# Performance work log

Measured on AMD Instinct MI355X. Metric: run time of the kernel, lower is better.

The kernel has to match this reference:

```python
import jax, jax.numpy as jnp
import numpy as np

V = 25
C = 3
EPS = 1e-5
# ntu_pairs (v1, v2): bone[v1-1] = x[v1-1] - x[v2-1]; each v1 appears exactly once
_PAIRS = ((1, 2), (2, 21), (3, 21), (4, 3), (5, 21), (6, 5), (7, 6), (8, 7), (9, 21),
          (10, 9), (11, 10), (12, 11), (13, 1), (14, 13), (15, 14), (16, 15), (17, 1),
          (18, 17), (19, 18), (20, 19), (22, 23), (21, 21), (23, 8), (24, 25), (25, 12))
_parent = np.zeros(V, dtype=np.int32)
for v1, v2 in _PAIRS:
    _parent[v1 - 1] = v2 - 1
PARENT = jnp.asarray(_parent)


def _embed(z, g, b, wa, ba, wb, bb):
    # z: (N, C, V, T); BatchNorm1d over flattened C*V channels (training-mode batch stats)
    N, c, v, T = z.shape
    zf = z.reshape(N, c * v, T)
    mean = zf.mean(axis=(0, 2), keepdims=True)
    var = zf.var(axis=(0, 2), keepdims=True)
    zn = (zf - mean) * jax.lax.rsqrt(var + EPS) * g[None, :, None] + b[None, :, None]
    zn = zn.reshape(N, c, v, T)
    h = jax.nn.relu(jnp.einsum('ncvt,oc->novt', zn, wa) + ba[None, :, None, None])
    return jax.nn.relu(jnp.einsum('nhvt,oh->novt', h, wb) + bb[None, :, None, None])


def reference(x, bn_g1, bn_b1, w1a, b1a, w1b, b1b, bn_g2, bn_b2, w2a, b2a, w2b, b2b):
    N, T, VC = x.shape
    xi = x.reshape(N, T, V, C).transpose(0, 3, 2, 1)  # (N, C, V, T)
    # fused gather-subtract replacing the 25-pair python loop
    bone = xi - xi[:, :, PARENT, :]
    # t_bone[..., :-1] = bone[..., 1:] - bone[..., :-1]; last frame zero
    t_bone = jnp.pad(bone[..., 1:] - bone[..., :-1], ((0, 0), (0, 0), (0, 0), (0, 1)))
    out = _embed(bone, bn_g1, bn_b1, w1a, b1a, w1b, b1b) + \
          _embed(t_bone, bn_g2, bn_b2, w2a, b2a, w2b, b2b)
    return out


def setup_inputs() -> dict:
    key = jax.random.key(0)
    ks = jax.random.split(key, 8)
    N, T = 256, 300
    return {
        'x': jax.random.normal(ks[0], (N, T, V * C), dtype=jnp.float32),
        'bn_g1': jnp.ones((V * C,), jnp.float32),
        'bn_b1': jnp.zeros((V * C,), jnp.float32),
        'w1a': jax.random.normal(ks[1], (64, C), jnp.float32) * 0.3,
        'b1a': jax.random.normal(ks[2], (64,), jnp.float32) * 0.1,
        'w1b': jax.random.normal(ks[3], (64, 64), jnp.float32) * 0.1,
        'b1b': jax.random.normal(ks[4], (64,), jnp.float32) * 0.1,
        'bn_g2': jnp.ones((V * C,), jnp.float32),
        'bn_b2': jnp.zeros((V * C,), jnp.float32),
        'w2a': jax.random.normal(ks[5], (64, C), jnp.float32) * 0.3,
        'b2a': jax.random.normal(ks[6], (64,), jnp.float32) * 0.1,
        'w2b': jax.random.normal(ks[7], (64, 64), jnp.float32) * 0.1,
        'b2b': jax.random.normal(jax.random.fold_in(key, 7), (64,), jnp.float32) * 0.1,
    }
```

## Files before the change

kernel.cpp:

```cpp
#include <hip/hip_runtime.h>
#include <stdint.h>


#define T_ 300

typedef __attribute__((ext_vector_type(8))) short bf16x8;
typedef __attribute__((ext_vector_type(4))) float f32x4;

__device__ __constant__ int PARENT_D[25] = {1,20,20,2,20,4,5,6,20,8,9,10,0,12,13,14,0,16,17,18,20,22,7,24,11};

static __device__ __forceinline__ unsigned short f2bf(float f) {
  unsigned int u = __float_as_uint(f);
  unsigned int r = (u + 0x7FFFu + ((u >> 16) & 1u)) >> 16;
  return (unsigned short)r;
}

__global__ void k0_zero(float* p, int cnt) {
  int i = blockIdx.x * blockDim.x + threadIdx.x;
  if (i < cnt) p[i] = 0.f;
}

__global__ void k1_stats(const float* __restrict__ x, float* __restrict__ stats) {
  __shared__ float rows[76 * 75];
  const int n = blockIdx.x;
  const int tid = threadIdx.x;
  float s0 = 0.f, s1 = 0.f, s2 = 0.f, s3 = 0.f;
  int j = tid, pj = 0, ch = 0;
  if (tid < 75) {
    int v = tid / 3, c = tid % 3;
    pj = PARENT_D[v] * 3 + c;
    ch = c * 25 + v;
  }
  const float* xb = x + (size_t)n * (T_ * 75);
  for (int chunk = 0; chunk < 4; ++chunk) {
    const int r0 = chunk * 75;
    const int nst = (chunk < 3) ? 76 : 75;
    __syncthreads();
    for (int i = tid; i < nst * 75; i += 256) rows[i] = xb[r0 * 75 + i];
    __syncthreads();
    if (tid < 75) {
      for (int r = 0; r < 75; ++r) {
        float b = rows[r * 75 + j] - rows[r * 75 + pj];
        s0 += b; s1 += b * b;
        if (r0 + r < 299) {
          float bn = rows[(r + 1) * 75 + j] - rows[(r + 1) * 75 + pj];
          float tb = bn - b;
          s2 += tb; s3 += tb * tb;
        }
      }
    }
  }
  if (tid < 75) {
    atomicAdd(&stats[ch * 2 + 0], s0);
    atomicAdd(&stats[ch * 2 + 1], s1);
    atomicAdd(&stats[150 + ch * 2 + 0], s2);
    atomicAdd(&stats[150 + ch * 2 + 1], s3);
  }
}

__global__ void k2_prep(const float* __restrict__ stats,
                        const float* __restrict__ g1, const float* __restrict__ bb1,
                        const float* __restrict__ w1a, const float* __restrict__ b1a,
                        const float* __restrict__ g2, const float* __restrict__ bb2,
                        const float* __restrict__ w2a, const float* __restrict__ b2a,
                        const float* __restrict__ w1b, const float* __restrict__ w2b,
                        unsigned short* __restrict__ wfA, unsigned short* __restrict__ wB) {
  __shared__ float sc[150], sh[150];
  const int tid = threadIdx.x;
  if (tid < 150) {
    int p = tid / 75, c75 = tid % 75;
    float s  = stats[p * 150 + c75 * 2 + 0];
    float sq = stats[p * 150 + c75 * 2 + 1];
    const float inv = 1.f / 76800.f;
    float mean = s * inv;
    float var = sq * inv - mean * mean;
    var = var < 0.f ? 0.f : var;
    float g  = (p ? g2 : g1)[c75];
    float bb = (p ? bb2 : bb1)[c75];
    float scale = g * rsqrtf(var + 1e-5f);
    sc[tid] = scale;
    sh[tid] = bb - mean * scale;
  }
  __syncthreads();
  for (int idx = tid; idx < 3200; idx += 256) {
    int p = idx / 1600, rm = idx % 1600, v = rm / 64, o = rm % 64;
    const float* wa = p ? w2a : w1a;
    const float* ba = p ? b2a : b1a;
    int base = p * 75;
    float sc0 = sc[base + v], sc1 = sc[base + 25 + v], sc2 = sc[base + 50 + v];
    float sh0 = sh[base + v], sh1 = sh[base + 25 + v], sh2 = sh[base + 50 + v];
    float a0 = wa[o * 3 + 0], a1 = wa[o * 3 + 1], a2 = wa[o * 3 + 2];
    float bias = ba[o] + a0 * sh0 + a1 * sh1 + a2 * sh2;
    unsigned short* d = wfA + (size_t)idx * 8;
    d[0] = f2bf(a0 * sc0); d[1] = f2bf(a1 * sc1); d[2] = f2bf(a2 * sc2);
    d[3] = f2bf(bias);
    d[4] = 0; d[5] = 0; d[6] = 0; d[7] = 0;
  }
  for (int idx = tid; idx < 8192; idx += 256)
    wB[idx] = f2bf(idx < 4096 ? w1b[idx] : w2b[idx - 4096]);
}

__launch_bounds__(256, 2)
__global__ void k3_main(const float* __restrict__ x,
                        const unsigned short* __restrict__ wfA,
                        const unsigned short* __restrict__ wB,
                        const float* __restrict__ b1b,
                        const float* __restrict__ b2b,
                        float* __restrict__ out) {
  __shared__ alignas(16) unsigned short Hs[4][32][72];
  const int tid = threadIdx.x;
  const int wave = tid >> 6;
  const int lane = tid & 63;
  const int q   = lane >> 4;
  const int l15 = lane & 15;
  const int p31 = lane & 31;

  const int wid = blockIdx.x * 4 + wave;
  const int chunk = wid % 10;
  const int rem = wid / 10;
  const int v = rem % 25;
  const int n = rem / 25;
  const int pv = PARENT_D[v];

  float b0 = 0.f, b1 = 0.f, b2 = 0.f, d0 = 0.f, d1 = 0.f, d2 = 0.f;
  if (lane < 32) {
    int t = chunk * 32 + p31;
    int t0 = t < 299 ? t : 299;
    int t1 = t + 1 < 299 ? t + 1 : 299;
    const float* r0 = x + (size_t)n * (T_ * 75) + t0 * 75;
    const float* r1 = x + (size_t)n * (T_ * 75) + t1 * 75;
    float xv0 = r0[v*3+0], xv1 = r0[v*3+1], xv2 = r0[v*3+2];
    float xp0 = r0[pv*3+0], xp1 = r0[pv*3+1], xp2 = r0[pv*3+2];
    float yv0 = r1[v*3+0], yv1 = r1[v*3+1], yv2 = r1[v*3+2];
    float yp0 = r1[pv*3+0], yp1 = r1[pv*3+1], yp2 = r1[pv*3+2];
    b0 = xv0 - xp0; b1 = xv1 - xp1; b2 = xv2 - xp2;
    d0 = (yv0 - yp0) - b0; d1 = (yv1 - yp1) - b1; d2 = (yv2 - yp2) - b2;
  }
  float b0s = __shfl(b0, 16 + l15), b1s = __shfl(b1, 16 + l15), b2s = __shfl(b2, 16 + l15);
  float d0s = __shfl(d0, 16 + l15), d1s = __shfl(d1, 16 + l15), d2s = __shfl(d2, 16 + l15);

  bf16x8 zf[2][2];
  {
    bf16x8 z8 = {0,0,0,0,0,0,0,0};
    zf[0][0] = z8; zf[0][1] = z8; zf[1][0] = z8; zf[1][1] = z8;
    if (q == 0) {
      zf[0][0][0]=(short)f2bf(b0);  zf[0][0][1]=(short)f2bf(b1);  zf[0][0][2]=(short)f2bf(b2);  zf[0][0][3]=(short)0x3F80;
      zf[0][1][0]=(short)f2bf(b0s); zf[0][1][1]=(short)f2bf(b1s); zf[0][1][2]=(short)f2bf(b2s); zf[0][1][3]=(short)0x3F80;
      zf[1][0][0]=(short)f2bf(d0);  zf[1][0][1]=(short)f2bf(d1);  zf[1][0][2]=(short)f2bf(d2);  zf[1][0][3]=(short)0x3F80;
      zf[1][1][0]=(short)f2bf(d0s); zf[1][1][1]=(short)f2bf(d1s); zf[1][1][2]=(short)f2bf(d2s); zf[1][1][3]=(short)0x3F80;
    }
  }

  bf16x8 wf[2][4];
#pragma unroll
  for (int p = 0; p < 2; ++p)
#pragma unroll
    for (int to = 0; to < 4; ++to) {
      bf16x8 w = {0,0,0,0,0,0,0,0};
      if (q == 0)
        w = *(const bf16x8*)(wfA + (size_t)((p * 25 + v) * 64 + l15 + 16 * to) * 8);
      wf[p][to] = w;
    }

  f32x4 acc[2][4][2];
  unsigned short (*Hrow)[72] = Hs[wave];

#pragma unroll
  for (int p = 0; p < 2; ++p) {
    f32x4 D[4][2];
#pragma unroll
    for (int to = 0; to < 4; ++to)
#pragma unroll
      for (int tc = 0; tc < 2; ++tc) {
        f32x4 z4 = {0.f, 0.f, 0.f, 0.f};
        D[to][tc] = __builtin_amdgcn_mfma_f32_16x16x32_bf16(wf[p][to], zf[p][tc], z4, 0, 0, 0);
      }
#pragma unroll
    for (int to = 0; to < 4; ++to)
#pragma unroll
      for (int tc = 0; tc < 2; ++tc) {
        f32x4 dd = D[to][tc];
        uint2 pk;
        pk.x = (unsigned)f2bf(fmaxf(dd[0], 0.f)) | ((unsigned)f2bf(fmaxf(dd[1], 0.f)) << 16);
        pk.y = (unsigned)f2bf(fmaxf(dd[2], 0.f)) | ((unsigned)f2bf(fmaxf(dd[3], 0.f)) << 16);
        *(uint2*)&Hrow[l15 + 16 * tc][16 * to + 4 * q] = pk;
      }
    asm volatile("s_waitcnt lgkmcnt(0)" ::: "memory");

    const unsigned short* wbp = wB + (size_t)p * 4096;
    const float* bias = p ? b2b : b1b;
#pragma unroll
    for (int to = 0; to < 4; ++to) {
      f32x4 bq = *(const f32x4*)(bias + 16 * to + 4 * q);
      acc[p][to][0] = bq;
      acc[p][to][1] = bq;
    }
#pragma unroll
    for (int ks = 0; ks < 2; ++ks) {
      bf16x8 wa2[4];
#pragma unroll
      for (int to = 0; to < 4; ++to)
        wa2[to] = *(const bf16x8*)(wbp + (l15 + 16 * to) * 64 + q * 8 + 32 * ks);
#pragma unroll
      for (int tc = 0; tc < 2; ++tc) {
        bf16x8 hb = *(const bf16x8*)&Hrow[l15 + 16 * tc][q * 8 + 32 * ks];
#pragma unroll
        for (int to = 0; to < 4; ++to)
          acc[p][to][tc] = __builtin_amdgcn_mfma_f32_16x16x32_bf16(wa2[to], hb, acc[p][to][tc], 0, 0, 0);
      }
    }
    asm volatile("s_waitcnt lgkmcnt(0)" ::: "memory");
  }

  const int tbase = chunk * 32;
#pragma unroll
  for (int tc = 0; tc < 2; ++tc) {
    int tpos = tbase + 16 * tc + l15;
    if (tpos < 300) {
#pragma unroll
      for (int to = 0; to < 4; ++to)
#pragma unroll
        for (int r = 0; r < 4; ++r) {
          int o = 16 * to + 4 * q + r;
          float val = fmaxf(acc[0][to][tc][r], 0.f) + fmaxf(acc[1][to][tc][r], 0.f);
          out[(((size_t)n * 64 + o) * 25 + v) * 300 + tpos] = val;
        }
    }
  }
}

extern "C" void kernel_launch(void* const* d_in, const int* in_sizes, int n_in,
                              void* d_out, int out_size, void* d_ws, size_t ws_size,
                              hipStream_t stream) {
  const float* x   = (const float*)d_in[0];
  const float* g1  = (const float*)d_in[1];
  const float* bb1 = (const float*)d_in[2];
  const float* w1a = (const float*)d_in[3];
  const float* b1a = (const float*)d_in[4];
  const float* w1b = (const float*)d_in[5];
  const float* b1b = (const float*)d_in[6];
  const float* g2  = (const float*)d_in[7];
  const float* bb2 = (const float*)d_in[8];
  const float* w2a = (const float*)d_in[9];
  const float* b2a = (const float*)d_in[10];
  const float* w2b = (const float*)d_in[11];
  const float* b2b = (const float*)d_in[12];

  float* stats = (float*)d_ws;
  unsigned short* wfA = (unsigned short*)((char*)d_ws + 2048);
  unsigned short* wB  = (unsigned short*)((char*)d_ws + 2048 + 51200);

  hipLaunchKernelGGL(k0_zero, dim3(2), dim3(256), 0, stream, stats, 512);
  hipLaunchKernelGGL(k1_stats, dim3(256), dim3(256), 0, stream, x, stats);
  hipLaunchKernelGGL(k2_prep, dim3(1), dim3(256), 0, stream, stats,
                     g1, bb1, w1a, b1a, g2, bb2, w2a, b2a, w1b, w2b, wfA, wB);
  hipLaunchKernelGGL(k3_main, dim3(16000), dim3(256), 0, stream, x, wfA, wB, b1b, b2b, (float*)d_out);
}
```

Baseline: 724.4 us.

## Split stats kernel over time slices and stage input rows in shared memory

The stats kernel now launches a 2D grid of batch times four time slices, each writing to its own partial-stats buffer. The prep kernel sums the four partials, which raises parallelism and reduces atomic contention. The main kernel is regrouped so one 320-thread block handles five joints of one (n, time-chunk). It loads the 33 needed input rows once into shared memory with float4 copies instead of each wave doing scattered global loads. This adds LDS use and a block barrier, and changes occupancy by dropping the two-blocks-per-SM launch bound hint.

```diff
diff --git a/kernel.cpp b/kernel.cpp
--- a/kernel.cpp
+++ b/kernel.cpp
@@ -23,38 +23,34 @@
 __global__ void k1_stats(const float* __restrict__ x, float* __restrict__ stats) {
   __shared__ float rows[76 * 75];
   const int n = blockIdx.x;
+  const int s = blockIdx.y;
   const int tid = threadIdx.x;
-  float s0 = 0.f, s1 = 0.f, s2 = 0.f, s3 = 0.f;
-  int j = tid, pj = 0, ch = 0;
+  const int r0 = s * 75;
+  const int nrows = (s < 3) ? 76 : 75;
+  const float* xb = x + (size_t)n * (T_ * 75) + (size_t)r0 * 75;
+  for (int i = tid; i < nrows * 75; i += 256) rows[i] = xb[i];
+  __syncthreads();
   if (tid < 75) {
-    int v = tid / 3, c = tid % 3;
-    pj = PARENT_D[v] * 3 + c;
-    ch = c * 25 + v;
-  }
-  const float* xb = x + (size_t)n * (T_ * 75);
-  for (int chunk = 0; chunk < 4; ++chunk) {
-    const int r0 = chunk * 75;
-    const int nst = (chunk < 3) ? 76 : 75;
-    __syncthreads();
-    for (int i = tid; i < nst * 75; i += 256) rows[i] = xb[r0 * 75 + i];
-    __syncthreads();
-    if (tid < 75) {
-      for (int r = 0; r < 75; ++r) {
-        float b = rows[r * 75 + j] - rows[r * 75 + pj];
-        s0 += b; s1 += b * b;
-        if (r0 + r < 299) {
-          float bn = rows[(r + 1) * 75 + j] - rows[(r + 1) * 75 + pj];
-          float tb = bn - b;
-          s2 += tb; s3 += tb * tb;
-        }
-      }
-    }
-  }
-  if (tid < 75) {
-    atomicAdd(&stats[ch * 2 + 0], s0);
-    atomicAdd(&stats[ch * 2 + 1], s1);
-    atomicAdd(&stats[150 + ch * 2 + 0], s2);
-    atomicAdd(&stats[150 + ch * 2 + 1], s3);
+    const int vv = tid / 3, cc = tid % 3;
+    const int pj = PARENT_D[vv] * 3 + cc;
+    const int j = tid;
+    const int chn = cc * 25 + vv;
+    float s0 = 0.f, s1 = 0.f, s2 = 0.f, s3 = 0.f;
+    float b = rows[j] - rows[pj];
+    for (int r = 0; r < 75; ++r) {
+      s0 += b; s1 += b * b;
+      if (r0 + r < 299) {
+        float bn = rows[(r + 1) * 75 + j] - rows[(r + 1) * 75 + pj];
+        float tb = bn - b;
+        s2 += tb; s3 += tb * tb;
+        b = bn;
+      }
+    }
+    float* sb = stats + (size_t)s * 304;
+    atomicAdd(&sb[chn * 2 + 0], s0);
+    atomicAdd(&sb[chn * 2 + 1], s1);
+    atomicAdd(&sb[150 + chn * 2 + 0], s2);
+    atomicAdd(&sb[150 + chn * 2 + 1], s3);
   }
 }
 
@@ -69,8 +65,11 @@
   const int tid = threadIdx.x;
   if (tid < 150) {
     int p = tid / 75, c75 = tid % 75;
-    float s  = stats[p * 150 + c75 * 2 + 0];
-    float sq = stats[p * 150 + c75 * 2 + 1];
+    float s = 0.f, sq = 0.f;
+    for (int k = 0; k < 4; ++k) {
+      s  += stats[k * 304 + p * 150 + c75 * 2 + 0];
+      sq += stats[k * 304 + p * 150 + c75 * 2 + 1];
+    }
     const float inv = 1.f / 76800.f;
     float mean = s * inv;
     float var = sq * inv - mean * mean;
@@ -100,14 +99,15 @@
     wB[idx] = f2bf(idx < 4096 ? w1b[idx] : w2b[idx - 4096]);
 }
 
-__launch_bounds__(256, 2)
+__launch_bounds__(320)
 __global__ void k3_main(const float* __restrict__ x,
                         const unsigned short* __restrict__ wfA,
                         const unsigned short* __restrict__ wB,
                         const float* __restrict__ b1b,
                         const float* __restrict__ b2b,
                         float* __restrict__ out) {
-  __shared__ alignas(16) unsigned short Hs[4][32][72];
+  __shared__ float Sx[33 * 75];
+  __shared__ alignas(16) unsigned short Hs[5][32][72];
   const int tid = threadIdx.x;
   const int wave = tid >> 6;
   const int lane = tid & 63;
@@ -115,20 +115,33 @@
   const int l15 = lane & 15;
   const int p31 = lane & 31;
 
-  const int wid = blockIdx.x * 4 + wave;
-  const int chunk = wid % 10;
-  const int rem = wid / 10;
-  const int v = rem % 25;
-  const int n = rem / 25;
+  const int bid = blockIdx.x;
+  const int chunk = bid % 10;
+  const int rem = bid / 10;
+  const int vg = rem % 5;
+  const int n = rem / 5;
+  const int v = vg * 5 + wave;
   const int pv = PARENT_D[v];
+  const int tbase = chunk * 32;
+  const int nrows = (chunk < 9) ? 33 : 12;
+
+  {
+    const float* xb = x + (size_t)n * (T_ * 75) + (size_t)tbase * 75;
+    const int total = nrows * 75;
+    const int f4 = total >> 2;
+    for (int i = tid; i < f4; i += 320)
+      ((float4*)Sx)[i] = ((const float4*)xb)[i];
+    if (tid < (total & 3)) Sx[(f4 << 2) + tid] = xb[(f4 << 2) + tid];
+  }
+  __syncthreads();
 
   float b0 = 0.f, b1 = 0.f, b2 = 0.f, d0 = 0.f, d1 = 0.f, d2 = 0.f;
   if (lane < 32) {
-    int t = chunk * 32 + p31;
-    int t0 = t < 299 ? t : 299;
-    int t1 = t + 1 < 299 ? t + 1 : 299;
-    const float* r0 = x + (size_t)n * (T_ * 75) + t0 * 75;
-    const float* r1 = x + (size_t)n * (T_ * 75) + t1 * 75;
+    int t = tbase + p31;
+    int tr0 = (t < 299 ? t : 299) - tbase;
+    int tr1 = (t + 1 < 299 ? t + 1 : 299) - tbase;
+    const float* r0 = Sx + tr0 * 75;
+    const float* r1 = Sx + tr1 * 75;
     float xv0 = r0[v*3+0], xv1 = r0[v*3+1], xv2 = r0[v*3+2];
     float xp0 = r0[pv*3+0], xp1 = r0[pv*3+1], xp2 = r0[pv*3+2];
     float yv0 = r1[v*3+0], yv1 = r1[v*3+1], yv2 = r1[v*3+2];
@@ -212,7 +225,6 @@
     asm volatile("s_waitcnt lgkmcnt(0)" ::: "memory");
   }
 
-  const int tbase = chunk * 32;
 #pragma unroll
   for (int tc = 0; tc < 2; ++tc) {
     int tpos = tbase + 16 * tc + l15;
@@ -247,12 +259,12 @@
   const float* b2b = (const float*)d_in[12];
 
   float* stats = (float*)d_ws;
-  unsigned short* wfA = (unsigned short*)((char*)d_ws + 2048);
-  unsigned short* wB  = (unsigned short*)((char*)d_ws + 2048 + 51200);
-
-  hipLaunchKernelGGL(k0_zero, dim3(2), dim3(256), 0, stream, stats, 512);
-  hipLaunchKernelGGL(k1_stats, dim3(256), dim3(256), 0, stream, x, stats);
+  unsigned short* wfA = (unsigned short*)((char*)d_ws + 4864);
+  unsigned short* wB  = (unsigned short*)((char*)d_ws + 4864 + 51200);
+
+  hipLaunchKernelGGL(k0_zero, dim3(5), dim3(256), 0, stream, stats, 1216);
+  hipLaunchKernelGGL(k1_stats, dim3(256, 4), dim3(256), 0, stream, x, stats);
   hipLaunchKernelGGL(k2_prep, dim3(1), dim3(256), 0, stream, stats,
                      g1, bb1, w1a, b1a, g2, bb2, w2a, b2a, w1b, w2b, wfA, wB);
-  hipLaunchKernelGGL(k3_main, dim3(16000), dim3(256), 0, stream, x, wfA, wB, b1b, b2b, (float*)d_out);
-}
+  hipLaunchKernelGGL(k3_main, dim3(12800), dim3(320), 0, stream, x, wfA, wB, b1b, b2b, (float*)d_out);
+}
```

New measurement: 756.3 us. +4.4%, slower.
